# Optimization experiments

Hardware: AMD Instinct MI355X
Metric: run time of the kernel (lower is better)

Reference implementation:

```python
import jax, jax.numpy as jnp
import numpy as np

D_MODEL = 1024
DEPTH = 1024

def setup_inputs() -> dict:
    key = jax.random.key(0)
    ks = jax.random.split(key, 7)
    scale = 1.0 / np.sqrt(D_MODEL)
    x = jax.random.normal(ks[0], (4, 2048, D_MODEL), dtype=jnp.float32)
    Wq = jax.random.normal(ks[1], (D_MODEL, DEPTH), dtype=jnp.float32) * scale
    Wk = jax.random.normal(ks[2], (D_MODEL, DEPTH), dtype=jnp.float32) * scale
    Wv = jax.random.normal(ks[3], (D_MODEL, DEPTH), dtype=jnp.float32) * scale
    bq = jnp.zeros((DEPTH,), dtype=jnp.float32)
    bk = jnp.zeros((DEPTH,), dtype=jnp.float32)
    bv = jnp.zeros((DEPTH,), dtype=jnp.float32)
    return {"x": x, "Wq": Wq, "bq": bq, "Wk": Wk, "bk": bk, "Wv": Wv, "bv": bv}

def reference(x, Wq, bq, Wk, bk, Wv, bv):
    # Q/K/V linear projections (Keras Dense: x @ W + b)
    q = jnp.einsum('bsd,de->bse', x, Wq) + bq  # [B,S,depth]
    k = jnp.einsum('bsd,de->bse', x, Wk) + bk
    v = jnp.einsum('bsd,de->bse', x, Wv) + bv
    d_k = jnp.asarray(q.shape[-1], dtype=q.dtype)
    scores = jnp.einsum('bse,bte->bst', q, k) / jnp.sqrt(d_k)  # [B,S,S]
    attn = jax.nn.softmax(scores, axis=-1)
    return jnp.einsum('bst,bte->bse', attn, v)  # [B,S,depth]
```

## Files before the change

### kernel.cpp

```cpp
#include <hip/hip_runtime.h>
#include <stdint.h>
#include <type_traits>

typedef unsigned short u16;
using short8  = __attribute__((ext_vector_type(8))) short;
using ushort8 = __attribute__((ext_vector_type(8))) unsigned short;
using floatx4 = __attribute__((ext_vector_type(4))) float;

#define IC(n) (std::integral_constant<int, (n)>())

__device__ __forceinline__ u16 f2bf(float f) {
    unsigned u = __float_as_uint(f);
    u += 0x7fff + ((u >> 16) & 1);
    return (u16)(u >> 16);
}
__device__ __forceinline__ float bf2f(u16 h) {
    return __uint_as_float(((unsigned)h) << 16);
}

__device__ __forceinline__ void gload_lds16(const void* g, void* l) {
    auto gp = reinterpret_cast<const __attribute__((address_space(1))) unsigned int*>(
        reinterpret_cast<uintptr_t>(g));
    auto lp = reinterpret_cast<__attribute__((address_space(3))) unsigned int*>(
        reinterpret_cast<uintptr_t>(l));
    __builtin_amdgcn_global_load_lds(gp, lp, 16, 0, 0);
}

__global__ __launch_bounds__(256) void cvt_f32_bf16_kernel(
        const float* __restrict__ in, u16* __restrict__ out) {
    long i = ((long)blockIdx.x * 256 + threadIdx.x) * 4;
    float4 v = *(const float4*)(in + i);
    ushort4 o;
    o.x = f2bf(v.x); o.y = f2bf(v.y); o.z = f2bf(v.z); o.w = f2bf(v.w);
    *(ushort4*)(out + i) = o;
}

__global__ __launch_bounds__(256) void wt_kernel(
        const float* __restrict__ W0, const float* __restrict__ W1, const float* __restrict__ W2,
        u16* __restrict__ O0, u16* __restrict__ O1, u16* __restrict__ O2) {
    const float* W = blockIdx.z == 0 ? W0 : blockIdx.z == 1 ? W1 : W2;
    u16* O = blockIdx.z == 0 ? O0 : blockIdx.z == 1 ? O1 : O2;
    __shared__ float t[32][33];
    const int cx = threadIdx.x & 31, ry = threadIdx.x >> 5;
    const int d0 = blockIdx.x * 32, e0 = blockIdx.y * 32;
#pragma unroll
    for (int i = 0; i < 4; i++) t[ry + i * 8][cx] = W[(long)(d0 + ry + i * 8) * 1024 + e0 + cx];
    __syncthreads();
#pragma unroll
    for (int i = 0; i < 4; i++) O[(long)(e0 + ry + i * 8) * 1024 + d0 + cx] = f2bf(t[cx][ry + i * 8]);
}

__global__ __launch_bounds__(256) void vt_kernel(
        const u16* __restrict__ V, u16* __restrict__ Vt) {
    const int b = blockIdx.z;
    const u16* v = V + (long)b * 2048 * 1024;
    u16* o = Vt + (long)b * 1024 * 2048;
    __shared__ u16 t[64][68];
    const int c4 = (threadIdx.x & 15) * 4, r = threadIdx.x >> 4;
    const int e0 = blockIdx.x * 64, t0 = blockIdx.y * 64;
#pragma unroll
    for (int i = 0; i < 4; i++)
        *(ushort4*)&t[r + i * 16][c4] =
            *(const ushort4*)(v + (long)(t0 + r + i * 16) * 1024 + e0 + c4);
    __syncthreads();
#pragma unroll
    for (int i = 0; i < 4; i++) {
        const int e = r + i * 16;
        ushort4 d;
        d.x = t[c4 + 0][e]; d.y = t[c4 + 1][e]; d.z = t[c4 + 2][e]; d.w = t[c4 + 3][e];
        *(ushort4*)(o + (long)(e0 + e) * 2048 + t0 + c4) = d;
    }
}

template <int MODE, int BNT>
__global__ __launch_bounds__(512) void gemm8_kernel(
        const u16* __restrict__ A, const u16* __restrict__ Bt,
        void* __restrict__ out0, void* __restrict__ out1, void* __restrict__ out2,
        const float* __restrict__ b0, const float* __restrict__ b1, const float* __restrict__ b2,
        int K, int N, long sAb, long sBb, long sCb, float scale)
{
    extern __shared__ u16 lds[];
    constexpr int DB   = (BNT == 256) ? 32768 : 24576;
    constexpr int FNH  = (BNT == 256) ? 2 : 1;
    constexpr int WCOL = (BNT == 256) ? 64 : 32;
    const int tid = threadIdx.x, lane = tid & 63, wid = tid >> 6;
    const int wm = wid >> 2, wn = wid & 3;
    const int l15 = lane & 15, hib = (lane >> 4) * 16;

    const int nbx = gridDim.x;
    const int nwg = nbx * gridDim.y;
    int lin = blockIdx.y * nbx + blockIdx.x;
    lin = (lin & 7) * (nwg >> 3) + (lin >> 3);
    const long m0 = (long)(lin / nbx) * 256;
    const long n0 = (long)(lin % nbx) * BNT;

    const u16* Ab = A + (long)blockIdx.z * sAb;
    const u16* Bb = Bt + (long)blockIdx.z * sBb;
    const long ldk = K;
    const int NT = K >> 6;

    auto stA = [&](int dbuf, int S, int kt) {
#pragma unroll
        for (int i = 0; i < 2; ++i) {
            const int rl = tid >> 3;
            const int R  = S * 64 + rl;
            const int cb = (tid & 7) * 16;
            const int scb = cb ^ ((R & 7) << 4);
            const u16* src = Ab + (m0 + i * 128 + R) * ldk + (long)kt * 64 + (scb >> 1);
            u16* dst = lds + dbuf * DB + i * 8192 + S * 4096 + wid * 512;
            gload_lds16(src, dst);
        }
    };
    auto stB = [&](int dbuf, int NHs, int kt) {
#pragma unroll
        for (int i = 0; i < 2; ++i) {
            const int c = i * 2 + (wid >> 2);
            const int h = c >> 1, rb = (c & 1) * 64;
            const int w = (wid & 3) * 64 + lane;
            const int r32 = w >> 3;
            const int R = rb + NHs * 32 + r32;
            const int cb = (w & 7) * 16;
            const int scb = cb ^ ((R & 7) << 4);
            const u16* src = Bb + (n0 + h * 128 + R) * ldk + (long)kt * 64 + (scb >> 1);
            u16* dst = lds + dbuf * DB + 16384 + h * 8192 + (rb + NHs * 32) * 64 + (wid & 3) * 512;
            gload_lds16(src, dst);
        }
    };
    auto stB128 = [&](int dbuf, int kt) {
#pragma unroll
        for (int i = 0; i < 2; ++i) {
            const int R = i * 64 + (tid >> 3);
            const int cb = (tid & 7) * 16;
            const int scb = cb ^ ((R & 7) << 4);
            const u16* src = Bb + (n0 + R) * ldk + (long)kt * 64 + (scb >> 1);
            u16* dst = lds + dbuf * DB + 16384 + i * 4096 + tid * 8;
            gload_lds16(src, dst);
        }
    };

    floatx4 acc[8][2 * FNH] = {};
    short8 afr[4][2], bfr[FNH][2];

    auto LA = [&](int dbuf, auto MHc) {
        constexpr int MH = decltype(MHc)::value;
        const char* reg = (const char*)(lds + dbuf * DB + wm * 8192);
#pragma unroll
        for (int fm = 0; fm < 4; ++fm)
#pragma unroll
            for (int ks = 0; ks < 2; ++ks) {
                const int r = MH * 64 + fm * 16 + l15;
                const int cb = ks * 64 + hib;
                afr[fm][ks] = *(const short8*)(reg + r * 128 + (cb ^ ((r & 7) << 4)));
            }
    };
    auto LB = [&](int dbuf, auto NHc) {
        constexpr int NH = decltype(NHc)::value;
        if constexpr (BNT == 256) {
            const char* reg = (const char*)(lds + dbuf * DB + 16384 + (wn >> 1) * 8192);
#pragma unroll
            for (int fn = 0; fn < 2; ++fn)
#pragma unroll
                for (int ks = 0; ks < 2; ++ks) {
                    const int r = (wn & 1) * 64 + NH * 32 + fn * 16 + l15;
                    const int cb = ks * 64 + hib;
                    bfr[fn][ks] = *(const short8*)(reg + r * 128 + (cb ^ ((r & 7) << 4)));
                }
        } else {
            const char* reg = (const char*)(lds + dbuf * DB + 16384);
#pragma unroll
            for (int ks = 0; ks < 2; ++ks) {
                const int r = wn * 32 + NH * 16 + l15;
                const int cb = ks * 64 + hib;
                bfr[0][ks] = *(const short8*)(reg + r * 128 + (cb ^ ((r & 7) << 4)));
            }
        }
    };
    auto MM = [&](auto MHc, auto NHc) {
        constexpr int MH = decltype(MHc)::value;
        constexpr int NH = decltype(NHc)::value;
        __builtin_amdgcn_s_setprio(1);
#pragma unroll
        for (int ks = 0; ks < 2; ++ks)
#pragma unroll
            for (int fm = 0; fm < 4; ++fm)
#pragma unroll
                for (int fn = 0; fn < FNH; ++fn)
                    acc[MH * 4 + fm][NH * FNH + fn] = __builtin_amdgcn_mfma_f32_16x16x32_bf16(
                        afr[fm][ks], bfr[fn][ks], acc[MH * 4 + fm][NH * FNH + fn], 0, 0, 0);
        __builtin_amdgcn_s_setprio(0);
    };

#define BAR() __builtin_amdgcn_s_barrier()

    if constexpr (BNT == 256) {
        stA(0, 0, 0); stA(0, 1, 0); stB(0, 0, 0); stB(0, 1, 0);
        stA(1, 0, 1); stB(1, 1, 1);
        asm volatile("s_waitcnt vmcnt(4)");
    } else {
        stA(0, 0, 0); stA(0, 1, 0); stB128(0, 0);
        stA(1, 0, 1);
        asm volatile("s_waitcnt vmcnt(2)");
    }
    BAR();

    auto pair = [&](auto LASTC, int kt0) {
        constexpr bool L = decltype(LASTC)::value;
        if constexpr (BNT == 256) {
            stA(1, 1, kt0 + 1); stB(1, 0, kt0 + 1);
            LA(0, IC(0)); LB(0, IC(0));
            BAR();
            MM(IC(0), IC(0));
            LB(0, IC(1));
            MM(IC(0), IC(1));
            LA(0, IC(1));
            BAR();
            if (!L) { stA(0, 0, kt0 + 2); stB(0, 1, kt0 + 2); }
            BAR();
            MM(IC(1), IC(1));
            LB(0, IC(0));
            MM(IC(1), IC(0));
            if (L) asm volatile("s_waitcnt vmcnt(0)");
            else   asm volatile("s_waitcnt vmcnt(4)");
            BAR();
            if (!L) { stA(0, 1, kt0 + 2); stB(0, 0, kt0 + 2); }
            LA(1, IC(0)); LB(1, IC(0));
            BAR();
            MM(IC(0), IC(0));
            LB(1, IC(1));
            MM(IC(0), IC(1));
            LA(1, IC(1));
            BAR();
            if (!L) { stA(1, 0, kt0 + 3); stB(1, 1, kt0 + 3); }
            BAR();
            MM(IC(1), IC(1));
            LB(1, IC(0));
            MM(IC(1), IC(0));
            if (L) asm volatile("s_waitcnt vmcnt(0)");
            else   asm volatile("s_waitcnt vmcnt(4)");
            BAR();
        } else {
            stA(1, 1, kt0 + 1); stB128(1, kt0 + 1);
            LA(0, IC(0)); LB(0, IC(0));
            BAR();
            MM(IC(0), IC(0));
            LB(0, IC(1));
            MM(IC(0), IC(1));
            LA(0, IC(1));
            BAR();
            if (!L) stA(0, 0, kt0 + 2);
            BAR();
            MM(IC(1), IC(1));
            LB(0, IC(0));
            MM(IC(1), IC(0));
            if (L) asm volatile("s_waitcnt vmcnt(0)");
            else   asm volatile("s_waitcnt vmcnt(2)");
            BAR();
            if (!L) { stA(0, 1, kt0 + 2); stB128(0, kt0 + 2); }
            LA(1, IC(0)); LB(1, IC(0));
            BAR();
            MM(IC(0), IC(0));
            LB(1, IC(1));
            MM(IC(0), IC(1));
            LA(1, IC(1));
            BAR();
            if (!L) stA(1, 0, kt0 + 3);
            BAR();
            MM(IC(1), IC(1));
            LB(1, IC(0));
            MM(IC(1), IC(0));
            if (L) asm volatile("s_waitcnt vmcnt(0)");
            else   asm volatile("s_waitcnt vmcnt(2)");
            BAR();
        }
    };

    const int NITER = NT >> 1;
    int it = 0;
    for (; it < NITER - 1; ++it) pair(std::false_type{}, 2 * it);
    pair(std::true_type{}, 2 * it);

#undef BAR

    const int cr = (lane >> 4) * 4, cc = l15;
    char* ldsB = (char*)lds;
    __syncthreads();
    if (MODE == 2) {
#pragma unroll
        for (int an = 0; an < 2 * FNH; ++an) {
            const int col = wn * WCOL + an * 16 + cc;
#pragma unroll
            for (int am = 0; am < 8; ++am) {
                const int row = wm * 128 + am * 16 + cr;
#pragma unroll
                for (int j = 0; j < 4; ++j)
                    *(float*)(ldsB + ((((row + j) * BNT + col) * 4) ^ (((row + j) & 7) << 4))) =
                        acc[am][an][j];
            }
        }
        __syncthreads();
        constexpr int NIT = 256 * BNT / 4 / 512;
        float* O = (float*)out0 + (long)blockIdx.z * sCb;
#pragma unroll
        for (int i = 0; i < NIT; ++i) {
            const int g4 = tid + i * 512;
            const int row = g4 >> 5;
            const int c4  = g4 & 31;
            float4 v = *(const float4*)(ldsB + ((g4 * 16) ^ ((row & 7) << 4)));
            *(float4*)(O + (m0 + row) * (long)N + n0 + c4 * 4) = v;
        }
    } else {
        const int sel = (MODE == 0) ? (int)(n0 >> 10) : 0;
        const float* bias = (MODE == 0) ? (sel == 0 ? b0 : sel == 1 ? b1 : b2) : nullptr;
        const long nc0 = n0 & 1023;
#pragma unroll
        for (int an = 0; an < 2 * FNH; ++an) {
            const int col = wn * WCOL + an * 16 + cc;
            const float bvv = (MODE == 0) ? bias[nc0 + col] : 0.f;
#pragma unroll
            for (int am = 0; am < 8; ++am) {
                const int row = wm * 128 + am * 16 + cr;
#pragma unroll
                for (int j = 0; j < 4; ++j) {
                    float v = acc[am][an][j];
                    if (MODE == 1) v *= scale;
                    v += bvv;
                    *(u16*)(ldsB + ((((row + j) * BNT + col) * 2) ^ (((row + j) & 7) << 4))) = f2bf(v);
                }
            }
        }
        __syncthreads();
        constexpr int NIT = 256 * BNT / 8 / 512;
        constexpr int RSH = (BNT == 256) ? 5 : 4;
#pragma unroll
        for (int i = 0; i < NIT; ++i) {
            const int g8 = tid + i * 512;
            const int row = g8 >> RSH;
            const int c8  = g8 & ((BNT >> 3) - 1);
            ushort8 v = *(const ushort8*)(ldsB + ((g8 * 16) ^ ((row & 7) << 4)));
            if (MODE == 0) {
                u16* O = (u16*)(sel == 0 ? out0 : sel == 1 ? out1 : out2);
                *(ushort8*)(O + (m0 + row) * 1024 + nc0 + c8 * 8) = v;
            } else {
                u16* O = (u16*)out0 + (long)blockIdx.z * sCb;
                *(ushort8*)(O + (m0 + row) * (long)N + n0 + c8 * 8) = v;
            }
        }
    }
}

__global__ __launch_bounds__(256) void softmax_kernel(u16* __restrict__ S) {
    u16* p = S + (long)blockIdx.x * 2048;
    const int tid = threadIdx.x;
    union { int4 q; u16 u[8]; } in;
    in.q = *(const int4*)(p + tid * 8);
    float v[8];
#pragma unroll
    for (int i = 0; i < 8; i++) v[i] = bf2f(in.u[i]);
    float mx = v[0];
#pragma unroll
    for (int i = 1; i < 8; i++) mx = fmaxf(mx, v[i]);
#pragma unroll
    for (int off = 32; off; off >>= 1) mx = fmaxf(mx, __shfl_xor(mx, off));
    __shared__ float red[8];
    if ((tid & 63) == 0) red[tid >> 6] = mx;
    __syncthreads();
    mx = fmaxf(fmaxf(red[0], red[1]), fmaxf(red[2], red[3]));
    float s = 0.f;
#pragma unroll
    for (int i = 0; i < 8; i++) { v[i] = __expf(v[i] - mx); s += v[i]; }
#pragma unroll
    for (int off = 32; off; off >>= 1) s += __shfl_xor(s, off);
    if ((tid & 63) == 0) red[4 + (tid >> 6)] = s;
    __syncthreads();
    s = red[4] + red[5] + red[6] + red[7];
    const float inv = 1.f / s;
    union { int4 q; u16 u[8]; } out;
#pragma unroll
    for (int i = 0; i < 8; i++) out.u[i] = f2bf(v[i] * inv);
    *(int4*)(p + tid * 8) = out.q;
}

extern "C" void kernel_launch(void* const* d_in, const int* in_sizes, int n_in,
                              void* d_out, int out_size, void* d_ws, size_t ws_size,
                              hipStream_t stream) {
    const float* x  = (const float*)d_in[0];
    const float* Wq = (const float*)d_in[1];
    const float* bq = (const float*)d_in[2];
    const float* Wk = (const float*)d_in[3];
    const float* bk = (const float*)d_in[4];
    const float* Wv = (const float*)d_in[5];
    const float* bv = (const float*)d_in[6];
    float* out = (float*)d_out;

    char* ws = (char*)d_ws;
    const long MB = 1L << 20;
    u16* xb = (u16*)(ws);
    u16* wt = (u16*)(ws + 16 * MB);
    u16* Q  = (u16*)(ws + 22 * MB);
    u16* Kb = (u16*)(ws + 38 * MB);
    u16* Vb = (u16*)(ws + 54 * MB);
    u16* Vt = (u16*)(ws + 70 * MB);
    u16* Sc = (u16*)(ws + 86 * MB);

    (void)hipFuncSetAttribute((const void*)gemm8_kernel<0, 128>, hipFuncAttributeMaxDynamicSharedMemorySize, 131072);
    (void)hipFuncSetAttribute((const void*)gemm8_kernel<1, 256>, hipFuncAttributeMaxDynamicSharedMemorySize, 131072);
    (void)hipFuncSetAttribute((const void*)gemm8_kernel<2, 128>, hipFuncAttributeMaxDynamicSharedMemorySize, 131072);

    cvt_f32_bf16_kernel<<<8192, 256, 0, stream>>>(x, xb);
    wt_kernel<<<dim3(32, 32, 3), 256, 0, stream>>>(Wq, Wk, Wv, wt, wt + 1024 * 1024, wt + 2 * 1024 * 1024);
    gemm8_kernel<0, 128><<<dim3(24, 32, 1), 512, 98304, stream>>>(
        xb, wt, Q, Kb, Vb, bq, bk, bv, 1024, 3072, 0, 0, 0, 1.f);
    vt_kernel<<<dim3(16, 32, 4), 256, 0, stream>>>(Vb, Vt);
    gemm8_kernel<1, 256><<<dim3(8, 8, 4), 512, 131072, stream>>>(
        Q, Kb, Sc, nullptr, nullptr, nullptr, nullptr, nullptr,
        1024, 2048, 2048L * 1024, 2048L * 1024, 2048L * 2048, 0.03125f);
    softmax_kernel<<<8192, 256, 0, stream>>>(Sc);
    gemm8_kernel<2, 128><<<dim3(8, 8, 4), 512, 131072, stream>>>(
        Sc, Vt, out, nullptr, nullptr, nullptr, nullptr, nullptr,
        2048, 1024, 2048L * 2048, 1024L * 2048, 2048L * 1024, 1.f);
}
```

Baseline: 180.9 us.

## Switch GEMM inner product from 16x16x32 to 32x32x16 bf16 MFMA tiles

Replaces the 16x16x32 MFMA fragments with 32x32x16 MFMA instructions, reorganizing the A/B fragment loads from LDS, the accumulator layout (floatx16 per 32x32 tile) and the epilogue row/column mapping. Larger MFMA tiles cut the number of LDS fragment reads per FLOP and the instruction count. Both B halves are now loaded up front, which raises register pressure and changes the overlap between LDS reads and MFMA issue.

```diff
diff --git a/kernel.cpp b/kernel.cpp
--- a/kernel.cpp
+++ b/kernel.cpp
@@ -3,9 +3,9 @@
 #include <type_traits>
 
 typedef unsigned short u16;
-using short8  = __attribute__((ext_vector_type(8))) short;
-using ushort8 = __attribute__((ext_vector_type(8))) unsigned short;
-using floatx4 = __attribute__((ext_vector_type(4))) float;
+using short8   = __attribute__((ext_vector_type(8))) short;
+using ushort8  = __attribute__((ext_vector_type(8))) unsigned short;
+using floatx16 = __attribute__((ext_vector_type(16))) float;
 
 #define IC(n) (std::integral_constant<int, (n)>())
 
@@ -81,11 +81,11 @@
 {
     extern __shared__ u16 lds[];
     constexpr int DB   = (BNT == 256) ? 32768 : 24576;
-    constexpr int FNH  = (BNT == 256) ? 2 : 1;
+    constexpr int NTL  = (BNT == 256) ? 2 : 1;
     constexpr int WCOL = (BNT == 256) ? 64 : 32;
     const int tid = threadIdx.x, lane = tid & 63, wid = tid >> 6;
     const int wm = wid >> 2, wn = wid & 3;
-    const int l15 = lane & 15, hib = (lane >> 4) * 16;
+    const int l31 = lane & 31, hk = (lane >> 5) * 16;
 
     const int nbx = gridDim.x;
     const int nwg = nbx * gridDim.y;
@@ -138,55 +138,45 @@
         }
     };
 
-    floatx4 acc[8][2 * FNH] = {};
-    short8 afr[4][2], bfr[FNH][2];
+    floatx16 acc[4][NTL] = {};
+    short8 a[2][4];
+    short8 b0f[4], b1f[4];
 
     auto LA = [&](int dbuf, auto MHc) {
         constexpr int MH = decltype(MHc)::value;
         const char* reg = (const char*)(lds + dbuf * DB + wm * 8192);
 #pragma unroll
-        for (int fm = 0; fm < 4; ++fm)
-#pragma unroll
-            for (int ks = 0; ks < 2; ++ks) {
-                const int r = MH * 64 + fm * 16 + l15;
-                const int cb = ks * 64 + hib;
-                afr[fm][ks] = *(const short8*)(reg + r * 128 + (cb ^ ((r & 7) << 4)));
+        for (int t = 0; t < 2; ++t)
+#pragma unroll
+            for (int s = 0; s < 4; ++s) {
+                const int r = MH * 64 + t * 32 + l31;
+                const int cb = s * 32 + hk;
+                a[t][s] = *(const short8*)(reg + r * 128 + (cb ^ ((r & 7) << 4)));
             }
     };
-    auto LB = [&](int dbuf, auto NHc) {
-        constexpr int NH = decltype(NHc)::value;
-        if constexpr (BNT == 256) {
-            const char* reg = (const char*)(lds + dbuf * DB + 16384 + (wn >> 1) * 8192);
-#pragma unroll
-            for (int fn = 0; fn < 2; ++fn)
-#pragma unroll
-                for (int ks = 0; ks < 2; ++ks) {
-                    const int r = (wn & 1) * 64 + NH * 32 + fn * 16 + l15;
-                    const int cb = ks * 64 + hib;
-                    bfr[fn][ks] = *(const short8*)(reg + r * 128 + (cb ^ ((r & 7) << 4)));
-                }
-        } else {
-            const char* reg = (const char*)(lds + dbuf * DB + 16384);
-#pragma unroll
-            for (int ks = 0; ks < 2; ++ks) {
-                const int r = wn * 32 + NH * 16 + l15;
-                const int cb = ks * 64 + hib;
-                bfr[0][ks] = *(const short8*)(reg + r * 128 + (cb ^ ((r & 7) << 4)));
-            }
-        }
-    };
-    auto MM = [&](auto MHc, auto NHc) {
+    auto LB = [&](int dbuf, auto NHc, short8 (&dst)[4]) {
+        const char* reg = (BNT == 256)
+            ? (const char*)(lds + dbuf * DB + 16384 + (wn >> 1) * 8192)
+            : (const char*)(lds + dbuf * DB + 16384);
+        const int rbase = (BNT == 256) ? ((wn & 1) * 64 + decltype(NHc)::value * 32)
+                                       : (wn * 32);
+#pragma unroll
+        for (int s = 0; s < 4; ++s) {
+            const int r = rbase + l31;
+            const int cb = s * 32 + hk;
+            dst[s] = *(const short8*)(reg + r * 128 + (cb ^ ((r & 7) << 4)));
+        }
+    };
+    auto MM = [&](short8 (&bf)[4], auto MHc, auto NHc) {
         constexpr int MH = decltype(MHc)::value;
         constexpr int NH = decltype(NHc)::value;
         __builtin_amdgcn_s_setprio(1);
 #pragma unroll
-        for (int ks = 0; ks < 2; ++ks)
-#pragma unroll
-            for (int fm = 0; fm < 4; ++fm)
-#pragma unroll
-                for (int fn = 0; fn < FNH; ++fn)
-                    acc[MH * 4 + fm][NH * FNH + fn] = __builtin_amdgcn_mfma_f32_16x16x32_bf16(
-                        afr[fm][ks], bfr[fn][ks], acc[MH * 4 + fm][NH * FNH + fn], 0, 0, 0);
+        for (int s = 0; s < 4; ++s)
+#pragma unroll
+            for (int t = 0; t < 2; ++t)
+                acc[MH * 2 + t][NH] = __builtin_amdgcn_mfma_f32_32x32x16_bf16(
+                    a[t][s], bf[s], acc[MH * 2 + t][NH], 0, 0, 0);
         __builtin_amdgcn_s_setprio(0);
     };
 
@@ -207,67 +197,55 @@
         constexpr bool L = decltype(LASTC)::value;
         if constexpr (BNT == 256) {
             stA(1, 1, kt0 + 1); stB(1, 0, kt0 + 1);
-            LA(0, IC(0)); LB(0, IC(0));
-            BAR();
-            MM(IC(0), IC(0));
-            LB(0, IC(1));
-            MM(IC(0), IC(1));
+            LA(0, IC(0)); LB(0, IC(0), b0f); LB(0, IC(1), b1f);
+            BAR();
+            MM(b0f, IC(0), IC(0));
+            MM(b1f, IC(0), IC(1));
             LA(0, IC(1));
             BAR();
             if (!L) { stA(0, 0, kt0 + 2); stB(0, 1, kt0 + 2); }
             BAR();
-            MM(IC(1), IC(1));
-            LB(0, IC(0));
-            MM(IC(1), IC(0));
+            MM(b1f, IC(1), IC(1));
+            MM(b0f, IC(1), IC(0));
             if (L) asm volatile("s_waitcnt vmcnt(0)");
             else   asm volatile("s_waitcnt vmcnt(4)");
             BAR();
             if (!L) { stA(0, 1, kt0 + 2); stB(0, 0, kt0 + 2); }
-            LA(1, IC(0)); LB(1, IC(0));
-            BAR();
-            MM(IC(0), IC(0));
-            LB(1, IC(1));
-            MM(IC(0), IC(1));
+            LA(1, IC(0)); LB(1, IC(0), b0f); LB(1, IC(1), b1f);
+            BAR();
+            MM(b0f, IC(0), IC(0));
+            MM(b1f, IC(0), IC(1));
             LA(1, IC(1));
             BAR();
             if (!L) { stA(1, 0, kt0 + 3); stB(1, 1, kt0 + 3); }
             BAR();
-            MM(IC(1), IC(1));
-            LB(1, IC(0));
-            MM(IC(1), IC(0));
+            MM(b1f, IC(1), IC(1));
+            MM(b0f, IC(1), IC(0));
             if (L) asm volatile("s_waitcnt vmcnt(0)");
             else   asm volatile("s_waitcnt vmcnt(4)");
             BAR();
         } else {
             stA(1, 1, kt0 + 1); stB128(1, kt0 + 1);
-            LA(0, IC(0)); LB(0, IC(0));
-            BAR();
-            MM(IC(0), IC(0));
-            LB(0, IC(1));
-            MM(IC(0), IC(1));
+            LA(0, IC(0)); LB(0, IC(0), b0f);
+            BAR();
+            MM(b0f, IC(0), IC(0));
             LA(0, IC(1));
             BAR();
             if (!L) stA(0, 0, kt0 + 2);
             BAR();
-            MM(IC(1), IC(1));
-            LB(0, IC(0));
-            MM(IC(1), IC(0));
+            MM(b0f, IC(1), IC(0));
             if (L) asm volatile("s_waitcnt vmcnt(0)");
             else   asm volatile("s_waitcnt vmcnt(2)");
             BAR();
             if (!L) { stA(0, 1, kt0 + 2); stB128(0, kt0 + 2); }
-            LA(1, IC(0)); LB(1, IC(0));
-            BAR();
-            MM(IC(0), IC(0));
-            LB(1, IC(1));
-            MM(IC(0), IC(1));
+            LA(1, IC(0)); LB(1, IC(0), b0f);
+            BAR();
+            MM(b0f, IC(0), IC(0));
             LA(1, IC(1));
             BAR();
             if (!L) stA(1, 0, kt0 + 3);
             BAR();
-            MM(IC(1), IC(1));
-            LB(1, IC(0));
-            MM(IC(1), IC(0));
+            MM(b0f, IC(1), IC(0));
             if (L) asm volatile("s_waitcnt vmcnt(0)");
             else   asm volatile("s_waitcnt vmcnt(2)");
             BAR();
@@ -281,21 +259,21 @@
 
 #undef BAR
 
-    const int cr = (lane >> 4) * 4, cc = l15;
     char* ldsB = (char*)lds;
     __syncthreads();
+    const int rh = (lane >> 5) * 4;
     if (MODE == 2) {
 #pragma unroll
-        for (int an = 0; an < 2 * FNH; ++an) {
-            const int col = wn * WCOL + an * 16 + cc;
-#pragma unroll
-            for (int am = 0; am < 8; ++am) {
-                const int row = wm * 128 + am * 16 + cr;
-#pragma unroll
-                for (int j = 0; j < 4; ++j)
-                    *(float*)(ldsB + ((((row + j) * BNT + col) * 4) ^ (((row + j) & 7) << 4))) =
-                        acc[am][an][j];
-            }
+        for (int nt = 0; nt < NTL; ++nt) {
+            const int col = wn * WCOL + nt * 32 + l31;
+#pragma unroll
+            for (int mt = 0; mt < 4; ++mt)
+#pragma unroll
+                for (int rg = 0; rg < 16; ++rg) {
+                    const int row = wm * 128 + mt * 32 + rh + (rg & 3) + ((rg >> 2) << 3);
+                    *(float*)(ldsB + (((row * BNT + col) * 4) ^ ((row & 7) << 4))) =
+                        acc[mt][nt][rg];
+                }
         }
         __syncthreads();
         constexpr int NIT = 256 * BNT / 4 / 512;
@@ -313,20 +291,19 @@
         const float* bias = (MODE == 0) ? (sel == 0 ? b0 : sel == 1 ? b1 : b2) : nullptr;
         const long nc0 = n0 & 1023;
 #pragma unroll
-        for (int an = 0; an < 2 * FNH; ++an) {
-            const int col = wn * WCOL + an * 16 + cc;
+        for (int nt = 0; nt < NTL; ++nt) {
+            const int col = wn * WCOL + nt * 32 + l31;
             const float bvv = (MODE == 0) ? bias[nc0 + col] : 0.f;
 #pragma unroll
-            for (int am = 0; am < 8; ++am) {
-                const int row = wm * 128 + am * 16 + cr;
-#pragma unroll
-                for (int j = 0; j < 4; ++j) {
-                    float v = acc[am][an][j];
+            for (int mt = 0; mt < 4; ++mt)
+#pragma unroll
+                for (int rg = 0; rg < 16; ++rg) {
+                    const int row = wm * 128 + mt * 32 + rh + (rg & 3) + ((rg >> 2) << 3);
+                    float v = acc[mt][nt][rg];
                     if (MODE == 1) v *= scale;
                     v += bvv;
-                    *(u16*)(ldsB + ((((row + j) * BNT + col) * 2) ^ (((row + j) & 7) << 4))) = f2bf(v);
+                    *(u16*)(ldsB + (((row * BNT + col) * 2) ^ ((row & 7) << 4))) = f2bf(v);
                 }
-            }
         }
         __syncthreads();
         constexpr int NIT = 256 * BNT / 8 / 512;
```

After: 193.8 us. 1.07x slower.
